# Kernel tuning notes

Measured on AMD Instinct MI355X. Metric: run time of the kernel, lower is better.

The kernel has to match this reference:

```python
import jax, jax.numpy as jnp
import numpy as np

DIM, HID, NC = 512, 102, 64
B, NS, ND, M = 256, 196, 196, 40
EPS_LN = 1e-5


def setup_inputs() -> dict:
    key = jax.random.key(0)
    ks = jax.random.split(key, 8)
    s = lambda d: 1.0 / np.sqrt(d)
    return {
        "tokens_sparse": jax.random.normal(ks[0], (B, NS, DIM), jnp.float32),
        "tokens_dense": jax.random.normal(ks[1], (B, ND, DIM), jnp.float32),
        "words": jax.random.normal(ks[2], (B, M, DIM), jnp.float32),
        "ln_g_s": jnp.ones((DIM,), jnp.float32),
        "ln_b_s": jnp.zeros((DIM,), jnp.float32),
        "w1_s": jax.random.normal(ks[3], (DIM, HID), jnp.float32) * s(DIM),
        "b1_s": jnp.zeros((HID,), jnp.float32),
        "w2_s": jax.random.normal(ks[4], (HID, NC), jnp.float32) * s(HID),
        "b2_s": jnp.zeros((NC,), jnp.float32),
        "ln_g_d": jnp.ones((DIM,), jnp.float32),
        "ln_b_d": jnp.zeros((DIM,), jnp.float32),
        "w1_d": jax.random.normal(ks[5], (DIM, HID), jnp.float32) * s(DIM),
        "b1_d": jnp.zeros((HID,), jnp.float32),
        "w2_d": jax.random.normal(ks[6], (HID, NC), jnp.float32) * s(HID),
        "b2_d": jnp.zeros((NC,), jnp.float32),
        "scale": jnp.ones((1, 1, 1), jnp.float32),
    }


def _layernorm(x, g, b):
    mu = x.mean(-1, keepdims=True)
    var = ((x - mu) ** 2).mean(-1, keepdims=True)
    return (x - mu) * jax.lax.rsqrt(var + EPS_LN) * g + b


def _aggregate(x, ln_g, ln_b, w1, b1, w2, b2, scale):
    # weight = MLP(LN(x)) -> (B, N, NC); transpose -> (B, NC, N); softmax over N; bmm
    h = jax.nn.gelu(_layernorm(x, ln_g, ln_b) @ w1 + b1, approximate=False)
    w = jnp.swapaxes(h @ w2 + b2, 1, 2) * scale            # (B, NC, N)
    w = jax.nn.softmax(w, axis=2)
    return jnp.einsum("bkn,bnc->bkc", w, x)                 # (B, NC, C)


def _l2norm(x):
    return x / jnp.maximum(jnp.linalg.norm(x, axis=-1, keepdims=True), 1e-8)


def reference(tokens_sparse, tokens_dense, words,
              ln_g_s, ln_b_s, w1_s, b1_s, w2_s, b2_s,
              ln_g_d, ln_b_d, w1_d, b1_d, w2_d, b2_d, scale):
    # DualTokenAggregation: paper Eq.(4)
    agg = _aggregate(tokens_sparse, ln_g_s, ln_b_s, w1_s, b1_s, w2_s, b2_s, scale)
    agg = agg + _aggregate(tokens_dense, ln_g_d, ln_b_d, w1_d, b1_d, w2_d, b2_d, scale)
    v = _l2norm(agg)                                        # (B, NC, C)
    t = _l2norm(words)                                      # (B, M, C)
    # HRPA (scan=True, bidirectional, no mask): bmm + leaky_relu + max/mean pooling
    sim = jnp.einsum("bmc,bkc->bmk", t, v)                  # (B, M, NC)
    sim = jnp.where(sim >= 0, sim, 0.1 * sim)               # leaky_relu(0.1)
    row_mean = sim.max(axis=2).mean(axis=1, keepdims=True)  # word->patch
    col_mean = sim.max(axis=1).mean(axis=1, keepdims=True)  # patch->word
    return row_mean + col_mean                              # (B, 1)
```

## Files before the change

### kernel.cpp

```cpp
#include <hip/hip_runtime.h>
#include <hip/hip_fp16.h>
#include <math.h>

#define Bb 256
#define Nn 196
#define Dd 512
#define Hh 102
#define Kk 64
#define Mm 40

#define LOGITS_BYTES 25690112
#define W1H_OFF  ((size_t)25690112)
#define W1L_OFF  (W1H_OFF + 262144)
#define GWB1_OFF (W1L_OFF + 262144)
#define W2TH_OFF (GWB1_OFF + 2048)
#define W2TL_OFF (W2TH_OFF + 32768)
#define AGG_OFF  (W2TL_OFF + 32768)

using short8 = __attribute__((ext_vector_type(8))) short;
using f32x4  = __attribute__((ext_vector_type(4))) float;

__device__ __forceinline__ void barrier_lgkm_only() {
  asm volatile("s_waitcnt lgkmcnt(0)" ::: "memory");
  __builtin_amdgcn_s_barrier();
  asm volatile("" ::: "memory");
}

__device__ __forceinline__ float dot4(const float4 a, const float4 b) {
  return a.x*b.x + a.y*b.y + a.z*b.z + a.w*b.w;
}
__device__ __forceinline__ float4 ld4s(const float* p) { return *(const float4*)p; }
__device__ __forceinline__ float gelu1(float z) {
  return 0.5f * z * (1.f + erff(z * 0.70710678118f));
}
__device__ __forceinline__ unsigned short bf16hi(float v) {
  return (unsigned short)(__float_as_uint(v) >> 16);
}
__device__ __forceinline__ float hipart(float v) {
  return __uint_as_float(__float_as_uint(v) & 0xffff0000u);
}
__device__ __forceinline__ unsigned short f2h(float v) {
  __half h = __float2half(v);
  return *(unsigned short*)&h;
}
__device__ __forceinline__ float h2f(unsigned short u) {
  __half h = *(__half*)&u;
  return __half2float(h);
}
__device__ __forceinline__ void split8(const float4 va, const float4 vb,
                                       short8& hh, short8& ll) {
  hh[0] = (short)bf16hi(va.x); ll[0] = (short)bf16hi(va.x - hipart(va.x));
  hh[1] = (short)bf16hi(va.y); ll[1] = (short)bf16hi(va.y - hipart(va.y));
  hh[2] = (short)bf16hi(va.z); ll[2] = (short)bf16hi(va.z - hipart(va.z));
  hh[3] = (short)bf16hi(va.w); ll[3] = (short)bf16hi(va.w - hipart(va.w));
  hh[4] = (short)bf16hi(vb.x); ll[4] = (short)bf16hi(vb.x - hipart(vb.x));
  hh[5] = (short)bf16hi(vb.y); ll[5] = (short)bf16hi(vb.y - hipart(vb.y));
  hh[6] = (short)bf16hi(vb.z); ll[6] = (short)bf16hi(vb.z - hipart(vb.z));
  hh[7] = (short)bf16hi(vb.w); ll[7] = (short)bf16hi(vb.w - hipart(vb.w));
}
__device__ __forceinline__ float wave_reduce_sum(float v) {
#pragma unroll
  for (int o = 1; o < 64; o <<= 1) v += __shfl_xor(v, o, 64);
  return v;
}
__device__ __forceinline__ float wave_reduce_max(float v) {
#pragma unroll
  for (int o = 1; o < 64; o <<= 1) v = fmaxf(v, __shfl_xor(v, o, 64));
  return v;
}

__global__ __launch_bounds__(512) void k0_wprep(
    const float* __restrict__ g_s, const float* __restrict__ b_s,
    const float* __restrict__ w1_s, const float* __restrict__ b1_s,
    const float* __restrict__ w2_s,
    const float* __restrict__ g_d, const float* __restrict__ b_d,
    const float* __restrict__ w1_d, const float* __restrict__ b1_d,
    const float* __restrict__ w2_d,
    unsigned short* __restrict__ w1h, unsigned short* __restrict__ w1l,
    float* __restrict__ gwb1,
    unsigned short* __restrict__ w2th, unsigned short* __restrict__ w2tl)
{
  const int p = blockIdx.x, slice = blockIdx.y;
  const float* g  = p ? g_d  : g_s;
  const float* bb = p ? b_d  : b_s;
  const float* w1 = p ? w1_d : w1_s;
  const float* b1 = p ? b1_d : b1_s;
  const float* w2 = p ? w2_d : w2_s;
  const int tid = threadIdx.x;

  if (slice < 8) {
    for (int idx = slice * 8192 + tid; idx < slice * 8192 + 8192; idx += 512) {
      const int j = idx & 127, c = idx >> 7;
      const float v = (j < Hh) ? w1[(size_t)c * Hh + j] * g[c] : 0.f;
      w1h[((size_t)(p * 128 + j)) * 512 + c] = bf16hi(v);
      w1l[((size_t)(p * 128 + j)) * 512 + c] = bf16hi(v - hipart(v));
    }
  } else {
    for (int idx = tid; idx < 8192; idx += 512) {
      const int k = idx >> 7, j = idx & 127;
      const float v = (j < Hh) ? w2[(size_t)j * Kk + k] : 0.f;
      w2th[(size_t)(p * 64 + k) * 128 + j] = bf16hi(v);
      w2tl[(size_t)(p * 64 + k) * 128 + j] = bf16hi(v - hipart(v));
    }
  }

  if (slice == 0) {
    __shared__ float red[4][128][2];
    const int j = tid & 127, part = tid >> 7;
    float sg = 0.f, sb = 0.f;
    if (j < Hh) {
      for (int c = part * 128; c < part * 128 + 128; ++c) {
        const float w = w1[(size_t)c * Hh + j];
        sg += g[c] * w;
        sb += bb[c] * w;
      }
    }
    red[part][j][0] = sg;
    red[part][j][1] = sb;
    __syncthreads();
    if (part == 0) {
      const float G  = red[0][j][0] + red[1][j][0] + red[2][j][0] + red[3][j][0];
      const float Bv = red[0][j][1] + red[1][j][1] + red[2][j][1] + red[3][j][1];
      gwb1[(p * 128 + j) * 2]     = G;
      gwb1[(p * 128 + j) * 2 + 1] = (j < Hh) ? (Bv + b1[j]) : 0.f;
    }
  }
}

__global__ __launch_bounds__(512) void k1_logits(
    const float* __restrict__ x_s, const float* __restrict__ x_d,
    const unsigned short* __restrict__ w1h, const unsigned short* __restrict__ w1l,
    const float* __restrict__ gwb1,
    const unsigned short* __restrict__ w2th, const unsigned short* __restrict__ w2tl,
    const float* __restrict__ b2_s, const float* __restrict__ b2_d,
    float* __restrict__ logits)
{
  __shared__ __align__(16) char smem1[40320];
  unsigned short* xbuf = (unsigned short*)smem1;
  unsigned short* hs_h = (unsigned short*)smem1;
  unsigned short* hs_l = (unsigned short*)(smem1 + 16128);
  float* part = (float*)(smem1 + 35840);
  float* st   = (float*)(smem1 + 39424);

  const int tid = threadIdx.x;
  const int ntile = blockIdx.x, p = blockIdx.y, b = blockIdx.z;
  const int nbase = ntile * 112;
  const float* x  = p ? x_d : x_s;
  const float* b2 = p ? b2_d : b2_s;

  const int lane = tid & 63, wv = tid >> 6;
  const int lr = lane & 15, lg = lane >> 4;
  const int jb = wv * 16;
  const unsigned short* wph = w1h + ((size_t)(p * 128 + jb + lr)) * 512 + lg * 8;
  const unsigned short* wpl = w1l + ((size_t)(p * 128 + jb + lr)) * 512 + lg * 8;

  const int t = tid >> 2, q = tid & 3;
  const bool stg = (tid < 448);
  const int n = nbase + t;
  const bool valid = stg && (n < Nn);
  const float* xrow = x + ((size_t)(b * Nn + (valid ? n : 0))) * Dd + q * 8;

  float psum = 0.f, psq = 0.f;
  f32x4 acc0 = {0,0,0,0}, acc1 = acc0, acc2 = acc0, acc3 = acc0;
  f32x4 acc4 = acc0, acc5 = acc0, acc6 = acc0;

  short8 bh_c = *(const short8*)(wph);
  short8 bl_c = *(const short8*)(wpl);

  {
    float4 va = {0,0,0,0}, vb = va;
    if (valid) { va = ld4s(xrow); vb = ld4s(xrow + 4); }
    if (stg) {
      psum += va.x + va.y + va.z + va.w + vb.x + vb.y + vb.z + vb.w;
      psq  += dot4(va, va) + dot4(vb, vb);
      short8 hh, ll;
      split8(va, vb, hh, ll);
      *(short8*)(xbuf + t * 40 + q * 8) = hh;
      *(short8*)(xbuf + 4480 + t * 40 + q * 8) = ll;
    }
  }
  float4 pva = {0,0,0,0}, pvb = pva;
  if (valid) { pva = ld4s(xrow + 32); pvb = ld4s(xrow + 36); }
  barrier_lgkm_only();

#pragma unroll 1
  for (int ch = 0; ch < 16; ++ch) {
    const int buf = ch & 1;
    const unsigned short* xh = xbuf + buf * 8960;
    const unsigned short* xl = xh + 4480;

    float4 nva = {0,0,0,0}, nvb = nva;
    if (ch < 14 && valid) {
      const int co = (ch + 2) * 32;
      nva = ld4s(xrow + co);
      nvb = ld4s(xrow + co + 4);
    }
    short8 bh_n = bh_c, bl_n = bl_c;
    if (ch < 15) {
      const int co = (ch + 1) * 32;
      bh_n = *(const short8*)(wph + co);
      bl_n = *(const short8*)(wpl + co);
    }

#define MSTEP(A, M) { \
    const short8 ah = *(const short8*)(xh + ((M) * 16 + lr) * 40 + lg * 8); \
    const short8 al = *(const short8*)(xl + ((M) * 16 + lr) * 40 + lg * 8); \
    (A) = __builtin_amdgcn_mfma_f32_16x16x32_bf16(ah, bh_c, (A), 0, 0, 0); \
    (A) = __builtin_amdgcn_mfma_f32_16x16x32_bf16(ah, bl_c, (A), 0, 0, 0); \
    (A) = __builtin_amdgcn_mfma_f32_16x16x32_bf16(al, bh_c, (A), 0, 0, 0); }
    MSTEP(acc0, 0) MSTEP(acc1, 1) MSTEP(acc2, 2) MSTEP(acc3, 3)
    MSTEP(acc4, 4) MSTEP(acc5, 5) MSTEP(acc6, 6)
#undef MSTEP

    if (ch < 15 && stg) {
      psum += pva.x + pva.y + pva.z + pva.w + pvb.x + pvb.y + pvb.z + pvb.w;
      psq  += dot4(pva, pva) + dot4(pvb, pvb);
      short8 hh, ll;
      split8(pva, pvb, hh, ll);
      unsigned short* xw = xbuf + (buf ^ 1) * 8960;
      *(short8*)(xw + t * 40 + q * 8) = hh;
      *(short8*)(xw + 4480 + t * 40 + q * 8) = ll;
    }
    pva = nva; pvb = nvb;
    bh_c = bh_n; bl_c = bl_n;
    barrier_lgkm_only();
  }

  if (stg) {
    part[t * 8 + q * 2]     = psum;
    part[t * 8 + q * 2 + 1] = psq;
  }
  __syncthreads();
  if (tid < 112) {
    const float s  = part[tid * 8] + part[tid * 8 + 2] + part[tid * 8 + 4] + part[tid * 8 + 6];
    const float ss = part[tid * 8 + 1] + part[tid * 8 + 3] + part[tid * 8 + 5] + part[tid * 8 + 7];
    const float mu  = s * (1.f / 512.f);
    const float var = fmaxf(ss * (1.f / 512.f) - mu * mu, 0.f);
    st[2 * tid]     = mu;
    st[2 * tid + 1] = rsqrtf(var + 1e-5f);
  }
  __syncthreads();

  const int colw = jb + lr;
  const float Gw = gwb1[(p * 128 + colw) * 2];
  const float B1 = gwb1[(p * 128 + colw) * 2 + 1];
  const int hwv  = wv >> 2;
  const int jloc = colw & 63;

#define HW1(A, M) { \
    _Pragma("unroll") \
    for (int rr = 0; rr < 4; ++rr) { \
      const int row = (M) * 16 + lg * 4 + rr; \
      const float mu = st[2 * row], rs = st[2 * row + 1]; \
      const float hv = gelu1(rs * (A)[rr] - mu * rs * Gw + B1); \
      hs_h[row * 72 + jloc] = bf16hi(hv); \
      hs_l[row * 72 + jloc] = bf16hi(hv - hipart(hv)); \
    } }
#define HWALL { HW1(acc0,0) HW1(acc1,1) HW1(acc2,2) HW1(acc3,3) \
                HW1(acc4,4) HW1(acc5,5) HW1(acc6,6) }

  f32x4 C0 = {0,0,0,0}, C1 = C0, C2 = C0, C3 = C0;
  const unsigned short* w2hb = w2th + (size_t)p * 8192 + lr * 128 + lg * 8;
  const unsigned short* w2lb = w2tl + (size_t)p * 8192 + lr * 128 + lg * 8;
  const int arow = (wv * 16 + lr) * 72 + lg * 8;

#define P2STEP(JG) { \
    const short8 Ah = *(const short8*)(hs_h + arow + ((JG) & 63)); \
    const short8 Al = *(const short8*)(hs_l + arow + ((JG) & 63)); \
    const short8 Bh0 = *(const short8*)(w2hb + (JG)); \
    const short8 Bl0 = *(const short8*)(w2lb + (JG)); \
    const short8 Bh1 = *(const short8*)(w2hb + 16 * 128 + (JG)); \
    const short8 Bl1 = *(const short8*)(w2lb + 16 * 128 + (JG)); \
    const short8 Bh2 = *(const short8*)(w2hb + 32 * 128 + (JG)); \
    const short8 Bl2 = *(const short8*)(w2lb + 32 * 128 + (JG)); \
    const short8 Bh3 = *(const short8*)(w2hb + 48 * 128 + (JG)); \
    const short8 Bl3 = *(const short8*)(w2lb + 48 * 128 + (JG)); \
    C0 = __builtin_amdgcn_mfma_f32_16x16x32_bf16(Ah, Bh0, C0, 0, 0, 0); \
    C0 = __builtin_amdgcn_mfma_f32_16x16x32_bf16(Ah, Bl0, C0, 0, 0, 0); \
    C0 = __builtin_amdgcn_mfma_f32_16x16x32_bf16(Al, Bh0, C0, 0, 0, 0); \
    C1 = __builtin_amdgcn_mfma_f32_16x16x32_bf16(Ah, Bh1, C1, 0, 0, 0); \
    C1 = __builtin_amdgcn_mfma_f32_16x16x32_bf16(Ah, Bl1, C1, 0, 0, 0); \
    C1 = __builtin_amdgcn_mfma_f32_16x16x32_bf16(Al, Bh1, C1, 0, 0, 0); \
    C2 = __builtin_amdgcn_mfma_f32_16x16x32_bf16(Ah, Bh2, C2, 0, 0, 0); \
    C2 = __builtin_amdgcn_mfma_f32_16x16x32_bf16(Ah, Bl2, C2, 0, 0, 0); \
    C2 = __builtin_amdgcn_mfma_f32_16x16x32_bf16(Al, Bh2, C2, 0, 0, 0); \
    C3 = __builtin_amdgcn_mfma_f32_16x16x32_bf16(Ah, Bh3, C3, 0, 0, 0); \
    C3 = __builtin_amdgcn_mfma_f32_16x16x32_bf16(Ah, Bl3, C3, 0, 0, 0); \
    C3 = __builtin_amdgcn_mfma_f32_16x16x32_bf16(Al, Bh3, C3, 0, 0, 0); }

  if (hwv == 0) { HWALL }
  __syncthreads();
  if (wv < 7) { P2STEP(0) P2STEP(32) }
  __syncthreads();
  if (hwv == 1) { HWALL }
  __syncthreads();
  if (wv < 7) { P2STEP(64) P2STEP(96) }
#undef P2STEP
#undef HWALL
#undef HW1

  if (wv < 7) {
    const float bb0 = b2[lr], bb1 = b2[16 + lr];
    const float bb2 = b2[32 + lr], bb3 = b2[48 + lr];
#pragma unroll
    for (int rr = 0; rr < 4; ++rr) {
      const int tok = wv * 16 + lg * 4 + rr;
      const int nn = nbase + tok;
      if (nn < Nn) {
        float* lgp = logits + ((size_t)(b * 2 + p) * Nn + nn) * Kk;
        lgp[lr]      = C0[rr] + bb0;
        lgp[16 + lr] = C1[rr] + bb1;
        lgp[32 + lr] = C2[rr] + bb2;
        lgp[48 + lr] = C3[rr] + bb3;
      }
    }
  }
}

__global__ __launch_bounds__(512) void k2_softmax_agg(
    const float* __restrict__ x_s, const float* __restrict__ x_d,
    const float* __restrict__ logits, const float* __restrict__ scale,
    unsigned short* __restrict__ aggP)
{
  __shared__ __align__(16) unsigned char smem2[68224];
  unsigned short* eh = (unsigned short*)smem2;
  unsigned short* el = (unsigned short*)(smem2 + 32768);
  float* rsk  = (float*)(smem2 + 65536);
  float* redf = (float*)(smem2 + 65792);
  float* mxk  = (float*)(smem2 + 67968);

  const int tid = threadIdx.x;
  const int p = blockIdx.x, b = blockIdx.y;
  const float sc = scale[0];
  const float* xb = (p ? x_d : x_s) + (size_t)b * Nn * Dd;

  const int kloc = tid & 63, sprt = tid >> 6;
  const float* lgp = logits + ((size_t)(b * 2 + p) * Nn) * Kk + kloc;
  const int eswz = (kloc & 31) << 3;
  float mx = -1e30f;
  for (int nn = sprt; nn < Nn; nn += 8) mx = fmaxf(mx, lgp[nn * 64] * sc);
  redf[sprt * 68 + kloc] = mx;
  __syncthreads();
  if (tid < 64) {
    float m = redf[tid];
#pragma unroll
    for (int gg = 1; gg < 8; ++gg) m = fmaxf(m, redf[gg * 68 + tid]);
    mxk[tid] = m;
  }
  __syncthreads();
  const float mk = mxk[kloc];
  float ssum = 0.f;
  for (int nn = sprt; nn < Nn; nn += 8) {
    const float e = expf(lgp[nn * 64] * sc - mk);
    const int ph = kloc * 256 + (nn ^ eswz);
    eh[ph] = bf16hi(e);
    el[ph] = bf16hi(e - hipart(e));
    ssum += e;
  }
  for (int nn = Nn + sprt; nn < 224; nn += 8) {
    const int ph = kloc * 256 + (nn ^ eswz);
    eh[ph] = 0; el[ph] = 0;
  }
  redf[sprt * 68 + kloc] = ssum;
  __syncthreads();
  if (tid < 64) {
    float s = 0.f;
#pragma unroll
    for (int gg = 0; gg < 8; ++gg) s += redf[gg * 68 + tid];
    rsk[tid] = 1.f / s;
  }
  __syncthreads();

  const int lane = tid & 63, wv = tid >> 6;
  const int lr = lane & 15, lg = lane >> 4;
  const int kt = wv & 3, ct = wv >> 2;
  const int arow = kt * 16 + lr;
  const int aswz = (arow & 31) << 3;
  const unsigned short* ebh = eh + arow * 256;
  const unsigned short* ebl = el + arow * 256;
  short8 Ah0, Ah1, Ah2, Ah3, Ah4, Ah5, Ah6;
  short8 Al0, Al1, Al2, Al3, Al4, Al5, Al6;
#define LDA(I) { const int off = ((I) * 32 + lg * 8) ^ aswz; \
  Ah##I = *(const short8*)(ebh + off); \
  Al##I = *(const short8*)(ebl + off); }
  LDA(0) LDA(1) LDA(2) LDA(3) LDA(4) LDA(5) LDA(6)
#undef LDA
  const int kbase = kt * 16 + lg * 4;
  const float r0 = rsk[kbase], r1 = rsk[kbase + 1];
  const float r2 = rsk[kbase + 2], r3 = rsk[kbase + 3];
  barrier_lgkm_only();

  const int brow = ct * 16 + lr;
  const int bswz = (brow & 31) << 3;
  const size_t agk = (size_t)((p * Bb + b) * Kk + kbase) * Dd;

#define K2STAGE(CHN, BUF) { \
    const int c0s = (CHN) * 32; \
    unsigned short* th = (unsigned short*)(smem2 + (BUF) * 32768); \
    unsigned short* tl = (unsigned short*)(smem2 + (BUF) * 32768 + 16384); \
    _Pragma("unroll") \
    for (int it = 0; it < 4; ++it) { \
      const int idx = it * 512 + tid; \
      const int cl = idx & 31, ngr = idx >> 5; \
      if (ngr < 56) { \
        const int n0 = ngr * 4; \
        const float* xpp = xb + (size_t)n0 * Dd + c0s + cl; \
        const float v0 = (n0     < Nn) ? xpp[0]      : 0.f; \
        const float v1 = (n0 + 1 < Nn) ? xpp[Dd]     : 0.f; \
        const float v2 = (n0 + 2 < Nn) ? xpp[2 * Dd] : 0.f; \
        const float v3 = (n0 + 3 < Nn) ? xpp[3 * Dd] : 0.f; \
        ushort4 hh4, ll4; \
        hh4.x = bf16hi(v0); ll4.x = bf16hi(v0 - hipart(v0)); \
        hh4.y = bf16hi(v1); ll4.y = bf16hi(v1 - hipart(v1)); \
        hh4.z = bf16hi(v2); ll4.z = bf16hi(v2 - hipart(v2)); \
        hh4.w = bf16hi(v3); ll4.w = bf16hi(v3 - hipart(v3)); \
        const int ph = cl * 256 + (n0 ^ ((cl & 31) << 3)); \
        *(ushort4*)(th + ph) = hh4; \
        *(ushort4*)(tl + ph) = ll4; \
      } \
    } }

  K2STAGE(0, 0)
  barrier_lgkm_only();

#pragma unroll 1
  for (int chn = 0; chn < 16; ++chn) {
    const int buf = chn & 1;
    if (chn < 15) { K2STAGE(chn + 1, buf ^ 1) }

    const unsigned short* bhb = (const unsigned short*)(smem2 + buf * 32768) + brow * 256;
    const unsigned short* blb = (const unsigned short*)(smem2 + buf * 32768 + 16384) + brow * 256;
    f32x4 acc = {0.f, 0.f, 0.f, 0.f};
#define K2KS(I) { \
    const int off = ((I) * 32 + lg * 8) ^ bswz; \
    const short8 Bh = *(const short8*)(bhb + off); \
    const short8 Bl = *(const short8*)(blb + off); \
    acc = __builtin_amdgcn_mfma_f32_16x16x32_bf16(Ah##I, Bh, acc, 0, 0, 0); \
    acc = __builtin_amdgcn_mfma_f32_16x16x32_bf16(Ah##I, Bl, acc, 0, 0, 0); \
    acc = __builtin_amdgcn_mfma_f32_16x16x32_bf16(Al##I, Bh, acc, 0, 0, 0); }
    K2KS(0) K2KS(1) K2KS(2) K2KS(3) K2KS(4) K2KS(5) K2KS(6)
#undef K2KS

    const int cc = chn * 32 + ct * 16 + lr;
    aggP[agk              + cc] = f2h(acc[0] * r0);
    aggP[agk +     (size_t)Dd + cc] = f2h(acc[1] * r1);
    aggP[agk + 2 * (size_t)Dd + cc] = f2h(acc[2] * r2);
    aggP[agk + 3 * (size_t)Dd + cc] = f2h(acc[3] * r3);
    barrier_lgkm_only();
  }
#undef K2STAGE
}

__global__ __launch_bounds__(512) void k4_final(
    const float* __restrict__ words, const unsigned short* __restrict__ aggP,
    float* __restrict__ outp)
{
  __shared__ __align__(16) unsigned char vls[64 * 512];
  __shared__ float rowm[40];
  __shared__ float colp[8][72];
  const int tid = threadIdx.x, b = blockIdx.x;
  const int w = tid >> 6, lane = tid & 63;
  const unsigned short* a0 = aggP + (size_t)b * (Kk * Dd);
  const unsigned short* a1 = aggP + ((size_t)(Bb + b)) * (Kk * Dd);
  const float* wrd = words + (size_t)b * Mm * Dd;
  const int m0 = w * 5;

  float rnt0, rnt1, rnt2, rnt3, rnt4;
#define TNORM(R, I) { \
    const float* tr = wrd + (size_t)(m0 + (I)) * Dd + lane * 8; \
    float4 ta = ld4s(tr), tb = ld4s(tr + 4); \
    float ss = wave_reduce_sum(dot4(ta, ta) + dot4(tb, tb)); \
    R = 1.f / fmaxf(sqrtf(ss), 1e-8f); }
  TNORM(rnt0, 0) TNORM(rnt1, 1) TNORM(rnt2, 2) TNORM(rnt3, 3) TNORM(rnt4, 4)
#undef TNORM

  float acc0 = 0.f, acc1 = 0.f, acc2 = 0.f, acc3 = 0.f, acc4 = 0.f, vsq = 0.f;

#pragma unroll 1
  for (int chn = 0; chn < 4; ++chn) {
    const int c0 = chn * 128;
    __syncthreads();
#pragma unroll
    for (int s = 0; s < 2; ++s) {
      const int idx = tid + s * 512;
      const int k = idx >> 4, g2 = idx & 15;
      const unsigned short* ph0 = a0 + (size_t)k * Dd + c0 + g2 * 8;
      const unsigned short* ph1 = a1 + (size_t)k * Dd + c0 + g2 * 8;
      const ushort4 u0a = *(const ushort4*)(ph0);
      const ushort4 u0b = *(const ushort4*)(ph0 + 4);
      const ushort4 u1a = *(const ushort4*)(ph1);
      const ushort4 u1b = *(const ushort4*)(ph1 + 4);
      float4 sa = {h2f(u0a.x) + h2f(u1a.x), h2f(u0a.y) + h2f(u1a.y),
                   h2f(u0a.z) + h2f(u1a.z), h2f(u0a.w) + h2f(u1a.w)};
      float4 sb = {h2f(u0b.x) + h2f(u1b.x), h2f(u0b.y) + h2f(u1b.y),
                   h2f(u0b.z) + h2f(u1b.z), h2f(u0b.w) + h2f(u1b.w)};
      const int gc0 = g2 * 2, gc1 = gc0 + 1;
      *(float4*)(vls + k * 512 + ((gc0 ^ (k & 31)) << 4)) = sa;
      *(float4*)(vls + k * 512 + ((gc1 ^ (k & 31)) << 4)) = sb;
    }
    __syncthreads();
#pragma unroll 2
    for (int cc = 0; cc < 32; ++cc) {
      const float4 vv = *(const float4*)(vls + lane * 512 + ((cc ^ (lane & 31)) << 4));
      const float* tp = wrd + c0 + cc * 4;
      const float4 t0 = ld4s(tp + (size_t)(m0    ) * Dd);
      const float4 t1 = ld4s(tp + (size_t)(m0 + 1) * Dd);
      const float4 t2 = ld4s(tp + (size_t)(m0 + 2) * Dd);
      const float4 t3 = ld4s(tp + (size_t)(m0 + 3) * Dd);
      const float4 t4 = ld4s(tp + (size_t)(m0 + 4) * Dd);
      acc0 += dot4(t0, vv); acc1 += dot4(t1, vv); acc2 += dot4(t2, vv);
      acc3 += dot4(t3, vv); acc4 += dot4(t4, vv);
      vsq  += dot4(vv, vv);
    }
  }

  const float rnv = 1.f / fmaxf(sqrtf(vsq), 1e-8f);
  float cmax = -1e30f;
#define DOM(ACC, RNT, I) { \
    float s = (ACC) * (RNT) * rnv; \
    s = (s >= 0.f) ? s : 0.1f * s; \
    cmax = fmaxf(cmax, s); \
    float rm = wave_reduce_max(s); \
    if (lane == 0) rowm[m0 + (I)] = rm; }
  DOM(acc0, rnt0, 0) DOM(acc1, rnt1, 1) DOM(acc2, rnt2, 2)
  DOM(acc3, rnt3, 3) DOM(acc4, rnt4, 4)
#undef DOM
  colp[w][lane] = cmax;
  __syncthreads();
  if (w == 0) {
    float cm = colp[0][lane];
#pragma unroll
    for (int ww = 1; ww < 8; ++ww) cm = fmaxf(cm, colp[ww][lane]);
    const float csum = wave_reduce_sum(cm);
    const float rv = (lane < 40) ? rowm[lane] : 0.f;
    const float rsum = wave_reduce_sum(rv);
    if (lane == 0) outp[b] = rsum * (1.f / 40.f) + csum * (1.f / 64.f);
  }
}

extern "C" void kernel_launch(void* const* d_in, const int* in_sizes, int n_in,
                              void* d_out, int out_size, void* d_ws, size_t ws_size,
                              hipStream_t stream)
{
  const float* x_s   = (const float*)d_in[0];
  const float* x_d   = (const float*)d_in[1];
  const float* words = (const float*)d_in[2];
  const float* g_s   = (const float*)d_in[3];
  const float* b_s   = (const float*)d_in[4];
  const float* w1_s  = (const float*)d_in[5];
  const float* b1_s  = (const float*)d_in[6];
  const float* w2_s  = (const float*)d_in[7];
  const float* b2_s  = (const float*)d_in[8];
  const float* g_d   = (const float*)d_in[9];
  const float* b_d   = (const float*)d_in[10];
  const float* w1_d  = (const float*)d_in[11];
  const float* b1_d  = (const float*)d_in[12];
  const float* w2_d  = (const float*)d_in[13];
  const float* b2_d  = (const float*)d_in[14];
  const float* scale = (const float*)d_in[15];
  (void)in_sizes; (void)n_in; (void)out_size; (void)ws_size;

  char* ws = (char*)d_ws;
  float* logits        = (float*)ws;
  unsigned short* w1h  = (unsigned short*)(ws + W1H_OFF);
  unsigned short* w1l  = (unsigned short*)(ws + W1L_OFF);
  float* gwb1          = (float*)(ws + GWB1_OFF);
  unsigned short* w2th = (unsigned short*)(ws + W2TH_OFF);
  unsigned short* w2tl = (unsigned short*)(ws + W2TL_OFF);
  unsigned short* aggP = (unsigned short*)(ws + AGG_OFF);

  hipLaunchKernelGGL(k0_wprep, dim3(2, 9), dim3(512), 0, stream,
                     g_s, b_s, w1_s, b1_s, w2_s, g_d, b_d, w1_d, b1_d, w2_d,
                     w1h, w1l, gwb1, w2th, w2tl);
  hipLaunchKernelGGL(k1_logits, dim3(2, 2, 256), dim3(512), 0, stream,
                     x_s, x_d, w1h, w1l, gwb1, w2th, w2tl,
                     b2_s, b2_d, logits);
  hipLaunchKernelGGL(k2_softmax_agg, dim3(2, Bb), dim3(512), 0, stream,
                     x_s, x_d, logits, scale, aggP);
  hipLaunchKernelGGL(k4_final, dim3(256), dim3(512), 0, stream,
                     words, aggP, (float*)d_out);
}
```

Measured before the change: 268.4 us.

## Split fused hidden-layer and logits GEMM kernel into two kernels via global buffer

```diff
diff --git a/kernel.cpp b/kernel.cpp
--- a/kernel.cpp
+++ b/kernel.cpp
@@ -15,7 +15,9 @@
 #define GWB1_OFF (W1L_OFF + 262144)
 #define W2TH_OFF (GWB1_OFF + 2048)
 #define W2TL_OFF (W2TH_OFF + 32768)
-#define AGG_OFF  (W2TL_OFF + 32768)
+#define H_OFF    (W2TL_OFF + 32768)
+#define HL_OFF   (H_OFF + 29360128)
+#define AGG_OFF  (HL_OFF + 29360128)
 
 using short8 = __attribute__((ext_vector_type(8))) short;
 using f32x4  = __attribute__((ext_vector_type(4))) float;
@@ -127,18 +129,14 @@
   }
 }
 
-__global__ __launch_bounds__(512) void k1_logits(
+__global__ __launch_bounds__(512) void k1a_hgemm(
     const float* __restrict__ x_s, const float* __restrict__ x_d,
     const unsigned short* __restrict__ w1h, const unsigned short* __restrict__ w1l,
     const float* __restrict__ gwb1,
-    const unsigned short* __restrict__ w2th, const unsigned short* __restrict__ w2tl,
-    const float* __restrict__ b2_s, const float* __restrict__ b2_d,
-    float* __restrict__ logits)
+    unsigned short* __restrict__ h_hi, unsigned short* __restrict__ h_lo)
 {
   __shared__ __align__(16) char smem1[40320];
   unsigned short* xbuf = (unsigned short*)smem1;
-  unsigned short* hs_h = (unsigned short*)smem1;
-  unsigned short* hs_l = (unsigned short*)(smem1 + 16128);
   float* part = (float*)(smem1 + 35840);
   float* st   = (float*)(smem1 + 39424);
 
@@ -146,7 +144,6 @@
   const int ntile = blockIdx.x, p = blockIdx.y, b = blockIdx.z;
   const int nbase = ntile * 112;
   const float* x  = p ? x_d : x_s;
-  const float* b2 = p ? b2_d : b2_s;
 
   const int lane = tid & 63, wv = tid >> 6;
   const int lr = lane & 15, lg = lane >> 4;
@@ -244,29 +241,45 @@
   const int colw = jb + lr;
   const float Gw = gwb1[(p * 128 + colw) * 2];
   const float B1 = gwb1[(p * 128 + colw) * 2 + 1];
-  const int hwv  = wv >> 2;
-  const int jloc = colw & 63;
-
+  const size_t hoff = (size_t)((b * 2 + p) * 2 + ntile) * 14336 + colw;
 #define HW1(A, M) { \
     _Pragma("unroll") \
     for (int rr = 0; rr < 4; ++rr) { \
       const int row = (M) * 16 + lg * 4 + rr; \
       const float mu = st[2 * row], rs = st[2 * row + 1]; \
       const float hv = gelu1(rs * (A)[rr] - mu * rs * Gw + B1); \
-      hs_h[row * 72 + jloc] = bf16hi(hv); \
-      hs_l[row * 72 + jloc] = bf16hi(hv - hipart(hv)); \
+      h_hi[hoff + row * 128] = bf16hi(hv); \
+      h_lo[hoff + row * 128] = bf16hi(hv - hipart(hv)); \
     } }
-#define HWALL { HW1(acc0,0) HW1(acc1,1) HW1(acc2,2) HW1(acc3,3) \
-                HW1(acc4,4) HW1(acc5,5) HW1(acc6,6) }
-
-  f32x4 C0 = {0,0,0,0}, C1 = C0, C2 = C0, C3 = C0;
+  HW1(acc0, 0) HW1(acc1, 1) HW1(acc2, 2) HW1(acc3, 3)
+  HW1(acc4, 4) HW1(acc5, 5) HW1(acc6, 6)
+#undef HW1
+}
+
+__global__ __launch_bounds__(448) void k1b_logits(
+    const unsigned short* __restrict__ h_hi, const unsigned short* __restrict__ h_lo,
+    const unsigned short* __restrict__ w2th, const unsigned short* __restrict__ w2tl,
+    const float* __restrict__ b2_s, const float* __restrict__ b2_d,
+    float* __restrict__ logits)
+{
+  const int tid = threadIdx.x;
+  const int ntile = blockIdx.x, p = blockIdx.y, b = blockIdx.z;
+  const int nbase = ntile * 112;
+  const float* b2 = p ? b2_d : b2_s;
+
+  const int lane = tid & 63, wv = tid >> 6;
+  const int lr = lane & 15, lg = lane >> 4;
+  const size_t hbase = (size_t)((b * 2 + p) * 2 + ntile) * 14336;
+  const unsigned short* hh = h_hi + hbase + (wv * 16 + lr) * 128 + lg * 8;
+  const unsigned short* hl = h_lo + hbase + (wv * 16 + lr) * 128 + lg * 8;
   const unsigned short* w2hb = w2th + (size_t)p * 8192 + lr * 128 + lg * 8;
   const unsigned short* w2lb = w2tl + (size_t)p * 8192 + lr * 128 + lg * 8;
-  const int arow = (wv * 16 + lr) * 72 + lg * 8;
+
+  f32x4 C0 = {0,0,0,0}, C1 = C0, C2 = C0, C3 = C0;
 
 #define P2STEP(JG) { \
-    const short8 Ah = *(const short8*)(hs_h + arow + ((JG) & 63)); \
-    const short8 Al = *(const short8*)(hs_l + arow + ((JG) & 63)); \
+    const short8 Ah = *(const short8*)(hh + (JG)); \
+    const short8 Al = *(const short8*)(hl + (JG)); \
     const short8 Bh0 = *(const short8*)(w2hb + (JG)); \
     const short8 Bl0 = *(const short8*)(w2lb + (JG)); \
     const short8 Bh1 = *(const short8*)(w2hb + 16 * 128 + (JG)); \
@@ -288,31 +301,21 @@
     C3 = __builtin_amdgcn_mfma_f32_16x16x32_bf16(Ah, Bl3, C3, 0, 0, 0); \
     C3 = __builtin_amdgcn_mfma_f32_16x16x32_bf16(Al, Bh3, C3, 0, 0, 0); }
 
-  if (hwv == 0) { HWALL }
-  __syncthreads();
-  if (wv < 7) { P2STEP(0) P2STEP(32) }
-  __syncthreads();
-  if (hwv == 1) { HWALL }
-  __syncthreads();
-  if (wv < 7) { P2STEP(64) P2STEP(96) }
+  P2STEP(0) P2STEP(32) P2STEP(64) P2STEP(96)
 #undef P2STEP
-#undef HWALL
-#undef HW1
-
-  if (wv < 7) {
-    const float bb0 = b2[lr], bb1 = b2[16 + lr];
-    const float bb2 = b2[32 + lr], bb3 = b2[48 + lr];
-#pragma unroll
-    for (int rr = 0; rr < 4; ++rr) {
-      const int tok = wv * 16 + lg * 4 + rr;
-      const int nn = nbase + tok;
-      if (nn < Nn) {
-        float* lgp = logits + ((size_t)(b * 2 + p) * Nn + nn) * Kk;
-        lgp[lr]      = C0[rr] + bb0;
-        lgp[16 + lr] = C1[rr] + bb1;
-        lgp[32 + lr] = C2[rr] + bb2;
-        lgp[48 + lr] = C3[rr] + bb3;
-      }
+
+  const float bb0 = b2[lr], bb1 = b2[16 + lr];
+  const float bb2 = b2[32 + lr], bb3 = b2[48 + lr];
+#pragma unroll
+  for (int rr = 0; rr < 4; ++rr) {
+    const int tok = wv * 16 + lg * 4 + rr;
+    const int nn = nbase + tok;
+    if (nn < Nn) {
+      float* lgp = logits + ((size_t)(b * 2 + p) * Nn + nn) * Kk;
+      lgp[lr]      = C0[rr] + bb0;
+      lgp[16 + lr] = C1[rr] + bb1;
+      lgp[32 + lr] = C2[rr] + bb2;
+      lgp[48 + lr] = C3[rr] + bb3;
     }
   }
 }
@@ -567,14 +570,17 @@
   float* gwb1          = (float*)(ws + GWB1_OFF);
   unsigned short* w2th = (unsigned short*)(ws + W2TH_OFF);
   unsigned short* w2tl = (unsigned short*)(ws + W2TL_OFF);
+  unsigned short* h_hi = (unsigned short*)(ws + H_OFF);
+  unsigned short* h_lo = (unsigned short*)(ws + HL_OFF);
   unsigned short* aggP = (unsigned short*)(ws + AGG_OFF);
 
   hipLaunchKernelGGL(k0_wprep, dim3(2, 9), dim3(512), 0, stream,
                      g_s, b_s, w1_s, b1_s, w2_s, g_d, b_d, w1_d, b1_d, w2_d,
                      w1h, w1l, gwb1, w2th, w2tl);
-  hipLaunchKernelGGL(k1_logits, dim3(2, 2, 256), dim3(512), 0, stream,
-                     x_s, x_d, w1h, w1l, gwb1, w2th, w2tl,
-                     b2_s, b2_d, logits);
+  hipLaunchKernelGGL(k1a_hgemm, dim3(2, 2, 256), dim3(512), 0, stream,
+                     x_s, x_d, w1h, w1l, gwb1, h_hi, h_lo);
+  hipLaunchKernelGGL(k1b_logits, dim3(2, 2, 256), dim3(448), 0, stream,
+                     h_hi, h_lo, w2th, w2tl, b2_s, b2_d, logits);
   hipLaunchKernelGGL(k2_softmax_agg, dim3(2, Bb), dim3(512), 0, stream,
                      x_s, x_d, logits, scale, aggP);
   hipLaunchKernelGGL(k4_final, dim3(256), dim3(512), 0, stream,
```

New measurement: 294.2 us. 9.6% more time.
